# Kernel optimization log

Measured on AMD Instinct MI355X. Metric: run time of the kernel, lower is better.

## Reference

```python
import jax, jax.numpy as jnp
import numpy as np

INPUT_DIM = 1024
OUTPUT_DIM = 512


def setup_inputs() -> dict:
    key = jax.random.key(0)
    ks = jax.random.split(key, 7)
    s_in = 1.0 / np.sqrt(INPUT_DIM)
    x = jax.random.normal(ks[0], (8, 2048, INPUT_DIM), dtype=jnp.float32)
    Wq = jax.random.uniform(ks[1], (INPUT_DIM, INPUT_DIM), jnp.float32, -s_in, s_in)
    bq = jax.random.uniform(ks[2], (INPUT_DIM,), jnp.float32, -s_in, s_in)
    Wk = jax.random.uniform(ks[3], (INPUT_DIM, INPUT_DIM), jnp.float32, -s_in, s_in)
    bk = jax.random.uniform(ks[4], (INPUT_DIM,), jnp.float32, -s_in, s_in)
    Wv = jax.random.uniform(ks[5], (INPUT_DIM, OUTPUT_DIM), jnp.float32, -s_in, s_in)
    bv = jax.random.uniform(ks[6], (OUTPUT_DIM,), jnp.float32, -s_in, s_in)
    return {"x": x, "Wq": Wq, "bq": bq, "Wk": Wk, "bk": bk, "Wv": Wv, "bv": bv}


def reference(x, Wq, bq, Wk, bk, Wv, bv):
    # x: [B, S, D]
    B, S, D = x.shape
    scale = 1.0 / jnp.sqrt(jnp.asarray(D, x.dtype))
    Q = jnp.einsum('bsd,de->bse', x, Wq) + bq  # [B,S,D]
    K = jnp.einsum('bsd,de->bse', x, Wk) + bk  # [B,S,D]
    V = jnp.einsum('bsd,de->bse', x, Wv) + bv  # [B,S,O]
    scores = jnp.einsum('bqd,bkd->bqk', Q, K) * scale  # [B,S,S]
    causal = jnp.tril(jnp.ones((S, S), dtype=bool))
    scores = jnp.where(causal, scores, -jnp.inf)
    attn = jax.nn.softmax(scores, axis=-1)
    return jnp.einsum('bqk,bko->bqo', attn, V)  # [B,S,O]
```

## Files before the change

kernel.cpp:

```cpp
#include <hip/hip_runtime.h>
#include <hip/hip_bf16.h>
#include <stdint.h>
#include <cmath>

typedef __bf16 bf16x8 __attribute__((ext_vector_type(8)));
typedef float f32x4 __attribute__((ext_vector_type(4)));

#define NB 8
#define NS 2048
#define ND 1024
#define NO 512

__device__ __forceinline__ unsigned short f2bf(float f) {
  union { float f; uint32_t u; } c;
  c.f = f;
  uint32_t u = c.u;
  uint32_t r = (u + 0x7fffu + ((u >> 16) & 1u)) >> 16;
  return (unsigned short)r;
}

__device__ __forceinline__ void glds16(const void* g, void* l) {
  __builtin_amdgcn_global_load_lds(
      (const __attribute__((address_space(1))) unsigned int*)g,
      (__attribute__((address_space(3))) unsigned int*)l, 16, 0, 0);
}

__global__ void cast_x_kernel(const float* __restrict__ in,
                              unsigned short* __restrict__ out, int n8) {
  int i = blockIdx.x * blockDim.x + threadIdx.x;
  if (i >= n8) return;
  const float4* p = reinterpret_cast<const float4*>(in) + 2 * (size_t)i;
  float4 a = p[0], b = p[1];
  union { unsigned short us[8]; int4 v; } r;
  r.us[0] = f2bf(a.x); r.us[1] = f2bf(a.y); r.us[2] = f2bf(a.z); r.us[3] = f2bf(a.w);
  r.us[4] = f2bf(b.x); r.us[5] = f2bf(b.y); r.us[6] = f2bf(b.z); r.us[7] = f2bf(b.w);
  reinterpret_cast<int4*>(out)[i] = r.v;
}

__global__ void transpose_cast_kernel(const float* __restrict__ in,
                                      unsigned short* __restrict__ out,
                                      int R, int C) {
  __shared__ unsigned short t[32][33];
  int bx = blockIdx.x;
  int by = blockIdx.y;
  int x = threadIdx.x & 31, y = threadIdx.x >> 5;
#pragma unroll
  for (int j = 0; j < 4; j++) {
    int r = by * 32 + y + j * 8;
    int c = bx * 32 + x;
    t[y + j * 8][x] = f2bf(in[(size_t)r * C + c]);
  }
  __syncthreads();
#pragma unroll
  for (int j = 0; j < 4; j++) {
    int c = bx * 32 + y + j * 8;
    int r = by * 32 + x;
    out[(size_t)c * R + r] = t[x][y + j * 8];
  }
}

__global__ void transpose_v_kernel(const unsigned short* __restrict__ in,
                                   unsigned short* __restrict__ out) {
  __shared__ unsigned short t[32][33];
  int b = blockIdx.z;
  int bo = blockIdx.x;
  int bs = blockIdx.y;
  const unsigned short* ib = in + (size_t)b * NS * NO;
  unsigned short* ob = out + (size_t)b * NO * NS;
  int x = threadIdx.x & 31, y = threadIdx.x >> 5;
#pragma unroll
  for (int j = 0; j < 4; j++)
    t[y + j * 8][x] = ib[(size_t)(bs * 32 + y + j * 8) * NO + bo * 32 + x];
  __syncthreads();
#pragma unroll
  for (int j = 0; j < 4; j++)
    ob[(size_t)(bo * 32 + y + j * 8) * NS + bs * 32 + x] = t[x][y + j * 8];
}

__global__ __launch_bounds__(256, 2) void gemm_bias_kernel(
    const unsigned short* __restrict__ A, const unsigned short* __restrict__ Bt,
    const float* __restrict__ bias, unsigned short* __restrict__ C,
    int M, int N, int K) {
  __shared__ unsigned short lA[128 * 32];
  __shared__ unsigned short lB[128 * 32];
  const int tid = threadIdx.x;
  const int w = tid >> 6, l = tid & 63;
  const int m0 = blockIdx.x * 128, n0 = blockIdx.y * 128;
  const int wr = w >> 1, wc = w & 1;
  const int lr16 = l & 15, lg = l >> 4;
  f32x4 acc[4][4];
#pragma unroll
  for (int i = 0; i < 4; i++)
#pragma unroll
    for (int j = 0; j < 4; j++) acc[i][j] = (f32x4){0.f, 0.f, 0.f, 0.f};
  const int srow = w * 32 + (l >> 2);
  const int sk = (l & 3) * 8;
  for (int k0 = 0; k0 < K; k0 += 32) {
#pragma unroll
    for (int j = 0; j < 2; j++) {
      glds16(&A[(size_t)(m0 + srow + j * 16) * K + k0 + sk], &lA[w * 1024 + j * 512]);
      glds16(&Bt[(size_t)(n0 + srow + j * 16) * K + k0 + sk], &lB[w * 1024 + j * 512]);
    }
    __syncthreads();
    bf16x8 af[4], bfr[4];
#pragma unroll
    for (int mi = 0; mi < 4; mi++)
      af[mi] = *reinterpret_cast<const bf16x8*>(&lA[(wr * 64 + mi * 16 + lr16) * 32 + lg * 8]);
#pragma unroll
    for (int ni = 0; ni < 4; ni++)
      bfr[ni] = *reinterpret_cast<const bf16x8*>(&lB[(wc * 64 + ni * 16 + lr16) * 32 + lg * 8]);
#pragma unroll
    for (int mi = 0; mi < 4; mi++)
#pragma unroll
      for (int ni = 0; ni < 4; ni++)
        acc[mi][ni] = __builtin_amdgcn_mfma_f32_16x16x32_bf16(af[mi], bfr[ni], acc[mi][ni], 0, 0, 0);
    __syncthreads();
  }
#pragma unroll
  for (int ni = 0; ni < 4; ni++) {
    int col = n0 + wc * 64 + ni * 16 + lr16;
    float bv = bias[col];
#pragma unroll
    for (int mi = 0; mi < 4; mi++) {
#pragma unroll
      for (int i = 0; i < 4; i++) {
        int row = m0 + wr * 64 + mi * 16 + lg * 4 + i;
        C[(size_t)row * N + col] = f2bf(acc[mi][ni][i] + bv);
      }
    }
  }
}

__global__ __launch_bounds__(256, 1) void flash_kernel(
    const unsigned short* __restrict__ Q, const unsigned short* __restrict__ K,
    const unsigned short* __restrict__ Vt, float* __restrict__ Out) {
  __shared__ unsigned short ubuf[3 * 8192];
  __shared__ unsigned short lP[64 * 64];
  const int bid = blockIdx.x;
  const int b = bid & 7, qi = bid >> 3;
  const int tid = threadIdx.x, w = tid >> 6, l = tid & 63;
  const unsigned short* Qb = Q + (size_t)b * NS * ND;
  const unsigned short* Kb = K + (size_t)b * NS * ND;
  const unsigned short* Vb = Vt + (size_t)b * NO * NS;
  float* Ob = Out + (size_t)b * NS * NO;
  const int q0 = qi * 64;
  const int lr16 = l & 15, lg = l >> 4;

  bf16x8 qreg[32];
  {
    const unsigned short* qrow = &Qb[(size_t)(q0 + w * 16 + lr16) * ND + lg * 8];
#pragma unroll
    for (int c = 0; c < 32; c++)
      qreg[c] = *reinterpret_cast<const bf16x8*>(qrow + c * 32);
  }

  f32x4 acc_o[32];
#pragma unroll
  for (int f = 0; f < 32; f++) acc_o[f] = (f32x4){0.f, 0.f, 0.f, 0.f};
  float m_s[4], l_s[4];
#pragma unroll
  for (int i = 0; i < 4; i++) { m_s[i] = -INFINITY; l_s[i] = 0.f; }
  const float sc = 0.03125f * 1.4426950408889634f;

  const int nkt = qi + 1;
  const int total = 12 * nkt;

  auto stage = [&](int g) {
    int ki = g / 12, u = g - ki * 12;
    int k0 = ki * 64;
    unsigned short* dst = &ubuf[(g % 3) * 8192];
    if (u < 8) {
#pragma unroll
      for (int j = 0; j < 4; j++) {
        int row = j * 16 + w * 4 + (l >> 4);
        int gl = (l & 15) ^ (row & 7);
        glds16(&Kb[(size_t)(k0 + row) * ND + u * 128 + gl * 8],
               dst + j * 2048 + w * 512);
      }
    } else {
      int nc = u - 8;
#pragma unroll
      for (int j = 0; j < 4; j++) {
        int row = j * 32 + w * 8 + (l >> 3);
        int gl = (l & 7) ^ (row & 7);
        glds16(&Vb[(size_t)(nc * 128 + row) * NS + k0 + gl * 8],
               dst + j * 2048 + w * 512);
      }
    }
  };

  stage(0);
  if (total > 1) stage(1);

  bf16x8 pa0 = {}, pa1 = {};
  for (int ki = 0; ki < nkt; ++ki) {
    const int k0 = ki * 64;
    const int gbase = ki * 12;
    f32x4 accs[4];
#pragma unroll
    for (int f = 0; f < 4; f++) accs[f] = (f32x4){0.f, 0.f, 0.f, 0.f};

#pragma unroll
    for (int u = 0; u < 12; ++u) {
      const int g = gbase + u;
      const bool isLast = (ki == nkt - 1) && (u == 11);
      if (!isLast)
        asm volatile("s_waitcnt vmcnt(4) lgkmcnt(0)\ns_barrier" ::: "memory");
      else
        asm volatile("s_waitcnt vmcnt(0) lgkmcnt(0)\ns_barrier" ::: "memory");
      if ((ki < nkt - 1) || (u < 10)) stage(g + 2);
      const unsigned short* bp = &ubuf[(g % 3) * 8192];

      if (u < 8) {
#pragma unroll
        for (int ks = 0; ks < 4; ks++) {
          bf16x8 a = qreg[u * 4 + ks];
#pragma unroll
          for (int fn = 0; fn < 4; fn++) {
            int row = fn * 16 + lr16;
            int p = (ks * 4 + lg) ^ (row & 7);
            bf16x8 bb = *reinterpret_cast<const bf16x8*>(&bp[row * 128 + p * 8]);
            accs[fn] = __builtin_amdgcn_mfma_f32_16x16x32_bf16(a, bb, accs[fn], 0, 0, 0);
          }
        }
        if (u == 7) {
          const bool diag = (ki == qi);
          float alpha[4];
#pragma unroll
          for (int i = 0; i < 4; i++) {
            float v0 = accs[0][i] * sc, v1 = accs[1][i] * sc;
            float v2 = accs[2][i] * sc, v3 = accs[3][i] * sc;
            if (diag) {
              int qr = w * 16 + lg * 4 + i;
              if (lr16 > qr) v0 = -INFINITY;
              if (16 + lr16 > qr) v1 = -INFINITY;
              if (32 + lr16 > qr) v2 = -INFINITY;
              if (48 + lr16 > qr) v3 = -INFINITY;
            }
            float pm = fmaxf(fmaxf(v0, v1), fmaxf(v2, v3));
            pm = fmaxf(pm, __shfl_xor(pm, 1));
            pm = fmaxf(pm, __shfl_xor(pm, 2));
            pm = fmaxf(pm, __shfl_xor(pm, 4));
            pm = fmaxf(pm, __shfl_xor(pm, 8));
            float mn = fmaxf(m_s[i], pm);
            float al = exp2f(m_s[i] - mn);
            float p0 = exp2f(v0 - mn), p1 = exp2f(v1 - mn);
            float p2 = exp2f(v2 - mn), p3 = exp2f(v3 - mn);
            float rs = (p0 + p1) + (p2 + p3);
            rs += __shfl_xor(rs, 1);
            rs += __shfl_xor(rs, 2);
            rs += __shfl_xor(rs, 4);
            rs += __shfl_xor(rs, 8);
            l_s[i] = l_s[i] * al + rs;
            m_s[i] = mn;
            alpha[i] = al;
            accs[0][i] = p0; accs[1][i] = p1; accs[2][i] = p2; accs[3][i] = p3;
          }
#pragma unroll
          for (int f = 0; f < 32; f++)
#pragma unroll
            for (int i = 0; i < 4; i++) acc_o[f][i] *= alpha[i];
#pragma unroll
          for (int fn = 0; fn < 4; fn++)
#pragma unroll
            for (int i = 0; i < 4; i++) {
              int pr = w * 16 + lg * 4 + i;
              int pg = (fn * 2 + (lr16 >> 3)) ^ (pr & 7);
              lP[pr * 64 + pg * 8 + (lr16 & 7)] = f2bf(accs[fn][i]);
            }
        }
      } else {
        const int nc = u - 8;
        if (u == 8) {
          int prow = w * 16 + lr16;
          pa0 = *reinterpret_cast<const bf16x8*>(&lP[prow * 64 + ((0 + lg) ^ (prow & 7)) * 8]);
          pa1 = *reinterpret_cast<const bf16x8*>(&lP[prow * 64 + ((4 + lg) ^ (prow & 7)) * 8]);
        }
#pragma unroll
        for (int fc = 0; fc < 8; fc++) {
          int row = fc * 16 + lr16;
          int p0i = (0 + lg) ^ (row & 7);
          int p1i = (4 + lg) ^ (row & 7);
          bf16x8 b0 = *reinterpret_cast<const bf16x8*>(&bp[row * 64 + p0i * 8]);
          bf16x8 b1 = *reinterpret_cast<const bf16x8*>(&bp[row * 64 + p1i * 8]);
          int f = nc * 8 + fc;
          acc_o[f] = __builtin_amdgcn_mfma_f32_16x16x32_bf16(pa0, b0, acc_o[f], 0, 0, 0);
          acc_o[f] = __builtin_amdgcn_mfma_f32_16x16x32_bf16(pa1, b1, acc_o[f], 0, 0, 0);
        }
      }
    }
  }

  float inv[4];
#pragma unroll
  for (int i = 0; i < 4; i++) inv[i] = 1.0f / l_s[i];
#pragma unroll
  for (int nc = 0; nc < 4; nc++)
#pragma unroll
    for (int fc = 0; fc < 8; fc++)
#pragma unroll
      for (int i = 0; i < 4; i++) {
        int row = q0 + w * 16 + lg * 4 + i;
        int col = nc * 128 + fc * 16 + lr16;
        Ob[(size_t)row * NO + col] = acc_o[nc * 8 + fc][i] * inv[i];
      }
}

extern "C" void kernel_launch(void* const* d_in, const int* in_sizes, int n_in,
                              void* d_out, int out_size, void* d_ws, size_t ws_size,
                              hipStream_t stream) {
  const float* x = (const float*)d_in[0];
  const float* Wq = (const float*)d_in[1];
  const float* bq = (const float*)d_in[2];
  const float* Wk = (const float*)d_in[3];
  const float* bk = (const float*)d_in[4];
  const float* Wv = (const float*)d_in[5];
  const float* bv = (const float*)d_in[6];
  float* out = (float*)d_out;
  char* ws = (char*)d_ws;

  unsigned short* xb  = (unsigned short*)(ws + 0);
  unsigned short* wqt = (unsigned short*)(ws + 33554432);
  unsigned short* wkt = (unsigned short*)(ws + 35651584);
  unsigned short* wvt = (unsigned short*)(ws + 37748736);
  unsigned short* Qb  = (unsigned short*)(ws + 38797312);
  unsigned short* Kb  = (unsigned short*)(ws + 72351744);
  unsigned short* Vb  = (unsigned short*)(ws + 105906176);
  unsigned short* Vtb = (unsigned short*)(ws + 122683392);

  cast_x_kernel<<<8192, 256, 0, stream>>>(x, xb, (NB * NS * ND) / 8);
  transpose_cast_kernel<<<dim3(32, 32), 256, 0, stream>>>(Wq, wqt, ND, ND);
  transpose_cast_kernel<<<dim3(32, 32), 256, 0, stream>>>(Wk, wkt, ND, ND);
  transpose_cast_kernel<<<dim3(16, 32), 256, 0, stream>>>(Wv, wvt, ND, NO);
  gemm_bias_kernel<<<dim3(128, 8), 256, 0, stream>>>(xb, wqt, bq, Qb, NB * NS, ND, ND);
  gemm_bias_kernel<<<dim3(128, 8), 256, 0, stream>>>(xb, wkt, bk, Kb, NB * NS, ND, ND);
  gemm_bias_kernel<<<dim3(128, 4), 256, 0, stream>>>(xb, wvt, bv, Vb, NB * NS, NO, ND);
  transpose_v_kernel<<<dim3(16, 64, 8), 256, 0, stream>>>(Vb, Vtb);
  flash_kernel<<<256, 256, 0, stream>>>(Qb, Kb, Vtb, out);
}
```

Baseline: 488.4 us.

## Split causal attention KV range across two blocks and merge partials

Result: slower. 599.6 us (+22.8%).

```diff
diff --git a/kernel.cpp b/kernel.cpp
--- a/kernel.cpp
+++ b/kernel.cpp
@@ -131,18 +131,28 @@
   }
 }
 
-__global__ __launch_bounds__(256, 1) void flash_kernel(
+__global__ __launch_bounds__(256, 2) void flash_split_kernel(
     const unsigned short* __restrict__ Q, const unsigned short* __restrict__ K,
-    const unsigned short* __restrict__ Vt, float* __restrict__ Out) {
+    const unsigned short* __restrict__ Vt, unsigned short* __restrict__ opart,
+    float* __restrict__ ml) {
   __shared__ unsigned short ubuf[3 * 8192];
   __shared__ unsigned short lP[64 * 64];
   const int bid = blockIdx.x;
-  const int b = bid & 7, qi = bid >> 3;
+  const int b = bid & 7;
+  const int t = bid >> 3;
+  int qi, half;
+  if (t < 32) { qi = 31 - (t >> 1); half = t & 1; }
+  else        { int u2 = t - 32; qi = u2 >> 1; half = u2 & 1; }
+  const int nkt = qi + 1;
+  const int h = (qi + 2) >> 1;
+  const int lo = half ? h : 0;
+  const int hi = half ? nkt : h;
+  const int total = 12 * (hi - lo);
+
   const int tid = threadIdx.x, w = tid >> 6, l = tid & 63;
   const unsigned short* Qb = Q + (size_t)b * NS * ND;
   const unsigned short* Kb = K + (size_t)b * NS * ND;
   const unsigned short* Vb = Vt + (size_t)b * NO * NS;
-  float* Ob = Out + (size_t)b * NS * NO;
   const int q0 = qi * 64;
   const int lr16 = l & 15, lg = l >> 4;
 
@@ -162,11 +172,8 @@
   for (int i = 0; i < 4; i++) { m_s[i] = -INFINITY; l_s[i] = 0.f; }
   const float sc = 0.03125f * 1.4426950408889634f;
 
-  const int nkt = qi + 1;
-  const int total = 12 * nkt;
-
   auto stage = [&](int g) {
-    int ki = g / 12, u = g - ki * 12;
+    int ki = lo + g / 12, u = g - (g / 12) * 12;
     int k0 = ki * 64;
     unsigned short* dst = &ubuf[(g % 3) * 8192];
     if (u < 8) {
@@ -189,121 +196,171 @@
     }
   };
 
-  stage(0);
-  if (total > 1) stage(1);
-
-  bf16x8 pa0 = {}, pa1 = {};
-  for (int ki = 0; ki < nkt; ++ki) {
-    const int k0 = ki * 64;
-    const int gbase = ki * 12;
-    f32x4 accs[4];
-#pragma unroll
-    for (int f = 0; f < 4; f++) accs[f] = (f32x4){0.f, 0.f, 0.f, 0.f};
-
-#pragma unroll
-    for (int u = 0; u < 12; ++u) {
-      const int g = gbase + u;
-      const bool isLast = (ki == nkt - 1) && (u == 11);
-      if (!isLast)
-        asm volatile("s_waitcnt vmcnt(4) lgkmcnt(0)\ns_barrier" ::: "memory");
-      else
-        asm volatile("s_waitcnt vmcnt(0) lgkmcnt(0)\ns_barrier" ::: "memory");
-      if ((ki < nkt - 1) || (u < 10)) stage(g + 2);
-      const unsigned short* bp = &ubuf[(g % 3) * 8192];
-
-      if (u < 8) {
-#pragma unroll
-        for (int ks = 0; ks < 4; ks++) {
-          bf16x8 a = qreg[u * 4 + ks];
-#pragma unroll
-          for (int fn = 0; fn < 4; fn++) {
-            int row = fn * 16 + lr16;
-            int p = (ks * 4 + lg) ^ (row & 7);
-            bf16x8 bb = *reinterpret_cast<const bf16x8*>(&bp[row * 128 + p * 8]);
-            accs[fn] = __builtin_amdgcn_mfma_f32_16x16x32_bf16(a, bb, accs[fn], 0, 0, 0);
+  if (total > 0) {
+    stage(0);
+    stage(1);
+
+    bf16x8 pa0 = {}, pa1 = {};
+    for (int ki = lo; ki < hi; ++ki) {
+      const int gbase = (ki - lo) * 12;
+      f32x4 accs[4];
+#pragma unroll
+      for (int f = 0; f < 4; f++) accs[f] = (f32x4){0.f, 0.f, 0.f, 0.f};
+
+#pragma unroll
+      for (int u = 0; u < 12; ++u) {
+        const int g = gbase + u;
+        const bool isLast = (g == total - 1);
+        if (!isLast)
+          asm volatile("s_waitcnt vmcnt(4) lgkmcnt(0)\ns_barrier" ::: "memory");
+        else
+          asm volatile("s_waitcnt vmcnt(0) lgkmcnt(0)\ns_barrier" ::: "memory");
+        if (g + 2 < total) stage(g + 2);
+        const unsigned short* bp = &ubuf[(g % 3) * 8192];
+
+        if (u < 8) {
+#pragma unroll
+          for (int ks = 0; ks < 4; ks++) {
+            bf16x8 a = qreg[u * 4 + ks];
+#pragma unroll
+            for (int fn = 0; fn < 4; fn++) {
+              int row = fn * 16 + lr16;
+              int p = (ks * 4 + lg) ^ (row & 7);
+              bf16x8 bb = *reinterpret_cast<const bf16x8*>(&bp[row * 128 + p * 8]);
+              accs[fn] = __builtin_amdgcn_mfma_f32_16x16x32_bf16(a, bb, accs[fn], 0, 0, 0);
+            }
           }
-        }
-        if (u == 7) {
-          const bool diag = (ki == qi);
-          float alpha[4];
-#pragma unroll
-          for (int i = 0; i < 4; i++) {
-            float v0 = accs[0][i] * sc, v1 = accs[1][i] * sc;
-            float v2 = accs[2][i] * sc, v3 = accs[3][i] * sc;
-            if (diag) {
-              int qr = w * 16 + lg * 4 + i;
-              if (lr16 > qr) v0 = -INFINITY;
-              if (16 + lr16 > qr) v1 = -INFINITY;
-              if (32 + lr16 > qr) v2 = -INFINITY;
-              if (48 + lr16 > qr) v3 = -INFINITY;
+          if (u == 7) {
+            const bool diag = (ki == qi);
+            float alpha[4];
+#pragma unroll
+            for (int i = 0; i < 4; i++) {
+              float v0 = accs[0][i] * sc, v1 = accs[1][i] * sc;
+              float v2 = accs[2][i] * sc, v3 = accs[3][i] * sc;
+              if (diag) {
+                int qr = w * 16 + lg * 4 + i;
+                if (lr16 > qr) v0 = -INFINITY;
+                if (16 + lr16 > qr) v1 = -INFINITY;
+                if (32 + lr16 > qr) v2 = -INFINITY;
+                if (48 + lr16 > qr) v3 = -INFINITY;
+              }
+              float pm = fmaxf(fmaxf(v0, v1), fmaxf(v2, v3));
+              pm = fmaxf(pm, __shfl_xor(pm, 1));
+              pm = fmaxf(pm, __shfl_xor(pm, 2));
+              pm = fmaxf(pm, __shfl_xor(pm, 4));
+              pm = fmaxf(pm, __shfl_xor(pm, 8));
+              float mn = fmaxf(m_s[i], pm);
+              float al = exp2f(m_s[i] - mn);
+              float p0 = exp2f(v0 - mn), p1 = exp2f(v1 - mn);
+              float p2 = exp2f(v2 - mn), p3 = exp2f(v3 - mn);
+              float rs = (p0 + p1) + (p2 + p3);
+              rs += __shfl_xor(rs, 1);
+              rs += __shfl_xor(rs, 2);
+              rs += __shfl_xor(rs, 4);
+              rs += __shfl_xor(rs, 8);
+              l_s[i] = l_s[i] * al + rs;
+              m_s[i] = mn;
+              alpha[i] = al;
+              accs[0][i] = p0; accs[1][i] = p1; accs[2][i] = p2; accs[3][i] = p3;
             }
-            float pm = fmaxf(fmaxf(v0, v1), fmaxf(v2, v3));
-            pm = fmaxf(pm, __shfl_xor(pm, 1));
-            pm = fmaxf(pm, __shfl_xor(pm, 2));
-            pm = fmaxf(pm, __shfl_xor(pm, 4));
-            pm = fmaxf(pm, __shfl_xor(pm, 8));
-            float mn = fmaxf(m_s[i], pm);
-            float al = exp2f(m_s[i] - mn);
-            float p0 = exp2f(v0 - mn), p1 = exp2f(v1 - mn);
-            float p2 = exp2f(v2 - mn), p3 = exp2f(v3 - mn);
-            float rs = (p0 + p1) + (p2 + p3);
-            rs += __shfl_xor(rs, 1);
-            rs += __shfl_xor(rs, 2);
-            rs += __shfl_xor(rs, 4);
-            rs += __shfl_xor(rs, 8);
-            l_s[i] = l_s[i] * al + rs;
-            m_s[i] = mn;
-            alpha[i] = al;
-            accs[0][i] = p0; accs[1][i] = p1; accs[2][i] = p2; accs[3][i] = p3;
+#pragma unroll
+            for (int f = 0; f < 32; f++)
+#pragma unroll
+              for (int i = 0; i < 4; i++) acc_o[f][i] *= alpha[i];
+#pragma unroll
+            for (int fn = 0; fn < 4; fn++)
+#pragma unroll
+              for (int i = 0; i < 4; i++) {
+                int pr = w * 16 + lg * 4 + i;
+                int pg = (fn * 2 + (lr16 >> 3)) ^ (pr & 7);
+                lP[pr * 64 + pg * 8 + (lr16 & 7)] = f2bf(accs[fn][i]);
+              }
           }
-#pragma unroll
-          for (int f = 0; f < 32; f++)
-#pragma unroll
-            for (int i = 0; i < 4; i++) acc_o[f][i] *= alpha[i];
-#pragma unroll
-          for (int fn = 0; fn < 4; fn++)
-#pragma unroll
-            for (int i = 0; i < 4; i++) {
-              int pr = w * 16 + lg * 4 + i;
-              int pg = (fn * 2 + (lr16 >> 3)) ^ (pr & 7);
-              lP[pr * 64 + pg * 8 + (lr16 & 7)] = f2bf(accs[fn][i]);
-            }
-        }
-      } else {
-        const int nc = u - 8;
-        if (u == 8) {
-          int prow = w * 16 + lr16;
-          pa0 = *reinterpret_cast<const bf16x8*>(&lP[prow * 64 + ((0 + lg) ^ (prow & 7)) * 8]);
-          pa1 = *reinterpret_cast<const bf16x8*>(&lP[prow * 64 + ((4 + lg) ^ (prow & 7)) * 8]);
-        }
-#pragma unroll
-        for (int fc = 0; fc < 8; fc++) {
-          int row = fc * 16 + lr16;
-          int p0i = (0 + lg) ^ (row & 7);
-          int p1i = (4 + lg) ^ (row & 7);
-          bf16x8 b0 = *reinterpret_cast<const bf16x8*>(&bp[row * 64 + p0i * 8]);
-          bf16x8 b1 = *reinterpret_cast<const bf16x8*>(&bp[row * 64 + p1i * 8]);
-          int f = nc * 8 + fc;
-          acc_o[f] = __builtin_amdgcn_mfma_f32_16x16x32_bf16(pa0, b0, acc_o[f], 0, 0, 0);
-          acc_o[f] = __builtin_amdgcn_mfma_f32_16x16x32_bf16(pa1, b1, acc_o[f], 0, 0, 0);
+        } else {
+          const int nc = u - 8;
+          if (u == 8) {
+            int prow = w * 16 + lr16;
+            pa0 = *reinterpret_cast<const bf16x8*>(&lP[prow * 64 + ((0 + lg) ^ (prow & 7)) * 8]);
+            pa1 = *reinterpret_cast<const bf16x8*>(&lP[prow * 64 + ((4 + lg) ^ (prow & 7)) * 8]);
+          }
+#pragma unroll
+          for (int fc = 0; fc < 8; fc++) {
+            int row = fc * 16 + lr16;
+            int p0i = (0 + lg) ^ (row & 7);
+            int p1i = (4 + lg) ^ (row & 7);
+            bf16x8 b0 = *reinterpret_cast<const bf16x8*>(&bp[row * 64 + p0i * 8]);
+            bf16x8 b1 = *reinterpret_cast<const bf16x8*>(&bp[row * 64 + p1i * 8]);
+            int f = nc * 8 + fc;
+            acc_o[f] = __builtin_amdgcn_mfma_f32_16x16x32_bf16(pa0, b0, acc_o[f], 0, 0, 0);
+            acc_o[f] = __builtin_amdgcn_mfma_f32_16x16x32_bf16(pa1, b1, acc_o[f], 0, 0, 0);
+          }
         }
       }
     }
   }
 
-  float inv[4];
-#pragma unroll
-  for (int i = 0; i < 4; i++) inv[i] = 1.0f / l_s[i];
+  const int slot = (qi * 2 + half) * 8 + b;
+  unsigned short* op = opart + (size_t)slot * 64 * 512;
 #pragma unroll
   for (int nc = 0; nc < 4; nc++)
 #pragma unroll
     for (int fc = 0; fc < 8; fc++)
 #pragma unroll
       for (int i = 0; i < 4; i++) {
-        int row = q0 + w * 16 + lg * 4 + i;
+        int row = w * 16 + lg * 4 + i;
         int col = nc * 128 + fc * 16 + lr16;
-        Ob[(size_t)row * NO + col] = acc_o[nc * 8 + fc][i] * inv[i];
+        op[(size_t)row * 512 + col] = f2bf(acc_o[nc * 8 + fc][i]);
       }
+  float* mlp = ml + slot * 128;
+  if (lr16 == 0) {
+#pragma unroll
+    for (int i = 0; i < 4; i++) {
+      int row = w * 16 + lg * 4 + i;
+      mlp[row] = m_s[i];
+      mlp[64 + row] = l_s[i];
+    }
+  }
+}
+
+__global__ __launch_bounds__(256) void combine_kernel(
+    const unsigned short* __restrict__ opart, const float* __restrict__ ml,
+    float* __restrict__ Out) {
+  const int bid = blockIdx.x;
+  const int b = bid & 7, qi = bid >> 3;
+  const int tid = threadIdx.x;
+  const int c8 = (tid & 63) * 8;
+  const int rbase = (tid >> 6) * 16;
+  const int sA = (qi * 2 + 0) * 8 + b;
+  const int sB = sA + 8;
+  const unsigned short* OA = opart + (size_t)sA * 32768;
+  const unsigned short* OB = opart + (size_t)sB * 32768;
+  const float* mlA = ml + sA * 128;
+  const float* mlB = ml + sB * 128;
+  float* ob = Out + ((size_t)b * NS + qi * 64) * NO;
+#pragma unroll
+  for (int rr = 0; rr < 16; rr++) {
+    int r = rbase + rr;
+    float mA = mlA[r], lA = mlA[64 + r];
+    float mB = mlB[r], lB = mlB[64 + r];
+    float m = fmaxf(mA, mB);
+    float eA = exp2f(mA - m);
+    float eB = (mB == -INFINITY) ? 0.f : exp2f(mB - m);
+    float inv = 1.0f / (eA * lA + eB * lB);
+    bf16x8 a = *reinterpret_cast<const bf16x8*>(&OA[(size_t)r * 512 + c8]);
+    bf16x8 bb = *reinterpret_cast<const bf16x8*>(&OB[(size_t)r * 512 + c8]);
+    float4 o0, o1;
+    o0.x = ((float)a[0] * eA + (float)bb[0] * eB) * inv;
+    o0.y = ((float)a[1] * eA + (float)bb[1] * eB) * inv;
+    o0.z = ((float)a[2] * eA + (float)bb[2] * eB) * inv;
+    o0.w = ((float)a[3] * eA + (float)bb[3] * eB) * inv;
+    o1.x = ((float)a[4] * eA + (float)bb[4] * eB) * inv;
+    o1.y = ((float)a[5] * eA + (float)bb[5] * eB) * inv;
+    o1.z = ((float)a[6] * eA + (float)bb[6] * eB) * inv;
+    o1.w = ((float)a[7] * eA + (float)bb[7] * eB) * inv;
+    float4* dst = reinterpret_cast<float4*>(&ob[(size_t)r * 512 + c8]);
+    dst[0] = o0;
+    dst[1] = o1;
+  }
 }
 
 extern "C" void kernel_launch(void* const* d_in, const int* in_sizes, int n_in,
@@ -327,6 +384,8 @@
   unsigned short* Kb  = (unsigned short*)(ws + 72351744);
   unsigned short* Vb  = (unsigned short*)(ws + 105906176);
   unsigned short* Vtb = (unsigned short*)(ws + 122683392);
+  unsigned short* opart = xb;
+  float* mlbuf = (float*)(ws + 105906176);
 
   cast_x_kernel<<<8192, 256, 0, stream>>>(x, xb, (NB * NS * ND) / 8);
   transpose_cast_kernel<<<dim3(32, 32), 256, 0, stream>>>(Wq, wqt, ND, ND);
@@ -336,5 +395,6 @@
   gemm_bias_kernel<<<dim3(128, 8), 256, 0, stream>>>(xb, wkt, bk, Kb, NB * NS, ND, ND);
   gemm_bias_kernel<<<dim3(128, 4), 256, 0, stream>>>(xb, wvt, bv, Vb, NB * NS, NO, ND);
   transpose_v_kernel<<<dim3(16, 64, 8), 256, 0, stream>>>(Vb, Vtb);
-  flash_kernel<<<256, 256, 0, stream>>>(Qb, Kb, Vtb, out);
-}
+  flash_split_kernel<<<512, 256, 0, stream>>>(Qb, Kb, Vtb, opart, mlbuf);
+  combine_kernel<<<256, 256, 0, stream>>>(opart, mlbuf, out);
+}
```
